# Kernel tuning notes

Hardware: AMD Instinct MI355X
Metric: run time of the kernel (lower is better)

The kernel has to match this reference:

```python
import jax, jax.numpy as jnp
import numpy as np

H = 64
IN_DIM = 32
N = 50000
E = 100000
B = 500


def setup_inputs() -> dict:
    key = jax.random.key(0)
    ks = jax.random.split(key, 16)
    def rn(k, shape, s=0.05):
        return jax.random.normal(k, shape, dtype=jnp.float32) * s
    inp = dict(
        nfeat=rn(ks[0], (N, IN_DIM), 1.0),
        efeat=rn(ks[1], (E, 5), 1.0),
        lin0_w=rn(ks[2], (IN_DIM, H)), lin0_b=jnp.zeros((H,), jnp.float32),
        ew1=rn(ks[3], (5, 128)), eb1=jnp.zeros((128,), jnp.float32),
        ew2=rn(ks[4], (128, H * H)), eb2=jnp.zeros((H * H,), jnp.float32),
        conv_b=jnp.zeros((H,), jnp.float32),
        gru_wih=rn(ks[5], (3 * H, H)), gru_whh=rn(ks[6], (3 * H, H)),
        gru_bih=jnp.zeros((3 * H,), jnp.float32), gru_bhh=jnp.zeros((3 * H,), jnp.float32),
        lstm_wih=rn(ks[7], (4 * H, 2 * H)), lstm_whh=rn(ks[8], (4 * H, H)),
        lstm_bih=jnp.zeros((4 * H,), jnp.float32), lstm_bhh=jnp.zeros((4 * H,), jnp.float32),
        fc1_w=rn(ks[9], (2 * H, H)), fc1_b=jnp.zeros((H,), jnp.float32),
        fc2_w=rn(ks[10], (H, 1)), fc2_b=jnp.zeros((1,), jnp.float32),
        src=jax.random.randint(ks[11], (E,), 0, N),
        dst=jax.random.randint(ks[12], (E,), 0, N),
        graph_id=jnp.arange(N) // (N // B),  # B graphs of equal size, sorted
        num_graphs=B,
    )
    return inp


def reference(nfeat, efeat, lin0_w, lin0_b, ew1, eb1, ew2, eb2, conv_b,
              gru_wih, gru_whh, gru_bih, gru_bhh,
              lstm_wih, lstm_whh, lstm_bih, lstm_bhh,
              fc1_w, fc1_b, fc2_w, fc2_b,
              src, dst, graph_id, num_graphs):
    n_nodes = nfeat.shape[0]
    # lin0 + relu
    h = jax.nn.relu(nfeat @ lin0_w + lin0_b)  # [N, H]
    # edge-conditioned weight matrices (same for all 3 iterations)
    We = (jax.nn.relu(efeat @ ew1 + eb1) @ ew2 + eb2).reshape(-1, H, H)  # [E, H, H]
    deg = jnp.maximum(
        jax.ops.segment_sum(jnp.ones(src.shape[0], jnp.float32), dst, num_segments=n_nodes), 1.0)
    for _ in range(3):
        # NNConv: gather src feats, per-edge matmul, scatter-mean at dst
        msg = jnp.einsum('eh,eho->eo', h[src], We)  # [E, H]
        agg = jax.ops.segment_sum(msg, dst, num_segments=n_nodes) / deg[:, None]
        m = jax.nn.relu(agg + conv_b)
        # GRU step (PyTorch gate order r,z,n)
        gi = m @ gru_wih.T + gru_bih
        gh = h @ gru_whh.T + gru_bhh
        r = jax.nn.sigmoid(gi[:, :H] + gh[:, :H])
        z = jax.nn.sigmoid(gi[:, H:2 * H] + gh[:, H:2 * H])
        n = jnp.tanh(gi[:, 2 * H:] + r * gh[:, 2 * H:])
        h = (1.0 - z) * n + z * h
    feat = h  # [N, H]
    # Set2Set pooling: 3 iters, 1-layer LSTM with input 2H
    q_star = jnp.zeros((num_graphs, 2 * H), jnp.float32)
    hh = jnp.zeros((num_graphs, H), jnp.float32)
    cc = jnp.zeros((num_graphs, H), jnp.float32)
    for _ in range(3):
        gates = q_star @ lstm_wih.T + lstm_bih + hh @ lstm_whh.T + lstm_bhh
        i = jax.nn.sigmoid(gates[:, :H])
        f = jax.nn.sigmoid(gates[:, H:2 * H])
        g = jnp.tanh(gates[:, 2 * H:3 * H])
        o = jax.nn.sigmoid(gates[:, 3 * H:])
        cc = f * cc + i * g
        hh = o * jnp.tanh(cc)
        q = hh  # [B, H]
        e = jnp.sum(feat * q[graph_id], axis=-1)  # [N]
        emax = jax.ops.segment_max(e, graph_id, num_segments=num_graphs)
        alpha = jnp.exp(e - emax[graph_id])
        denom = jax.ops.segment_sum(alpha, graph_id, num_segments=num_graphs)
        alpha = alpha / denom[graph_id]
        readout = jax.ops.segment_sum(alpha[:, None] * feat, graph_id, num_segments=num_graphs)
        q_star = jnp.concatenate([q, readout], axis=-1)  # [B, 2H]
    pred = jax.nn.relu(q_star @ fc1_w + fc1_b) @ fc2_w + fc2_b  # [B, 1]
    return pred.reshape(-1)
```

## Files before the change

kernel.cpp:

```cpp
#include <hip/hip_runtime.h>

#define HD 64
#define NNODE 50000
#define NEDGE 100000
#define NGR 500
#define NPG 100
#define EPAD 100352
#define NCH 66

typedef _Float16 f16;
typedef _Float16 f16x2 __attribute__((ext_vector_type(2)));
typedef _Float16 f16x8 __attribute__((ext_vector_type(8)));
typedef float f32x4 __attribute__((ext_vector_type(4)));

__device__ __forceinline__ float sigmoidf_(float x) { return 1.f / (1.f + __expf(-x)); }

#define G_NODE 12500
#define G_EMLP 392
#define G_GRU  48
#define G_T1   128
#define G_T2   64
#define G_IDX  392
#define G_ALL (G_NODE + G_EMLP + G_GRU + G_T1 + G_T2 + G_IDX)

__global__ __launch_bounds__(256) void k_prep_all(
    const float* __restrict__ nfeat, const float* __restrict__ lin0_w, const float* __restrict__ lin0_b,
    const float* __restrict__ efeat, const float* __restrict__ ew1, const float* __restrict__ eb1,
    const float* __restrict__ gwih, const float* __restrict__ gwhh,
    const float* __restrict__ lwih, const float* __restrict__ lwhh,
    const int* __restrict__ src, const int* __restrict__ dst,
    float* __restrict__ h, f16x2* __restrict__ uP,
    f16* __restrict__ gB1, f16* __restrict__ gB2,
    float* __restrict__ lwihT, float* __restrict__ lwhhT,
    int* __restrict__ srcP, int* __restrict__ dstP, int* __restrict__ cnt) {
    int bb = blockIdx.x;
    int t = threadIdx.x;
    if (bb < G_NODE) {
        int idx = bb * 256 + t;
        int n = idx >> 6, o = idx & 63;
        if (n >= NNODE) return;
        const float* nf = nfeat + n * 32;
        float acc = lin0_b[o];
#pragma unroll
        for (int i = 0; i < 32; i++) acc += nf[i] * lin0_w[i * 64 + o];
        h[idx] = fmaxf(acc, 0.f);
        return;
    }
    bb -= G_NODE;
    if (bb < G_EMLP) {
        __shared__ float sw[5 * 128];
        __shared__ float sb[128];
        for (int idx = t; idx < 640; idx += 256) sw[idx] = ew1[idx];
        if (t < 128) sb[t] = eb1[t];
        __syncthreads();
        int e = bb * 256 + t;
        bool valid = e < NEDGE;
        float ef[5];
#pragma unroll
        for (int i = 0; i < 5; i++) ef[i] = valid ? efeat[e * 5 + i] : 0.f;
#pragma unroll 2
        for (int c = 0; c < 64; c++) {
            float v[2];
#pragma unroll
            for (int s = 0; s < 2; s++) {
                int k = 2 * c + s;
                float acc = sb[k];
#pragma unroll
                for (int i = 0; i < 5; i++) acc += ef[i] * sw[i * 128 + k];
                v[s] = valid ? fmaxf(acc, 0.f) : 0.f;
            }
            f16x2 pv;
            pv[0] = (f16)v[0];
            pv[1] = (f16)v[1];
            uP[(size_t)c * EPAD + e] = pv;
        }
        return;
    }
    bb -= G_EMLP;
    if (bb < G_GRU) {
        int idx = bb * 256 + t;
        int cp = idx >> 6, k = idx & 63;
        int w = cp / 48, rem = cp % 48;
        int tg = rem >> 4, cc = rem & 15;
        int orow = tg * 64 + w * 16 + cc;
        gB1[idx] = (f16)gwih[orow * 64 + k];
        gB2[idx] = (f16)gwhh[orow * 64 + k];
        return;
    }
    bb -= G_GRU;
    if (bb < G_T1) {
        int idx = bb * 256 + t;
        int r = idx >> 7, c = idx & 127;
        lwihT[c * 256 + r] = lwih[idx];
        return;
    }
    bb -= G_T1;
    if (bb < G_T2) {
        int idx = bb * 256 + t;
        int r = idx >> 6, c = idx & 63;
        lwhhT[c * 256 + r] = lwhh[idx];
        return;
    }
    bb -= G_T2;
    {
        int e = bb * 256 + t;
        if (e >= EPAD) return;
        if (e < NEDGE) {
            int d = dst[e];
            srcP[e] = src[e];
            dstP[e] = d;
            atomicAdd(&cnt[d], 1);
        } else {
            srcP[e] = 0;
            dstP[e] = -1;
        }
    }
}

__global__ __launch_bounds__(256) void k_pack_b(const float* __restrict__ ew2,
                                                const float* __restrict__ eb2,
                                                f16* __restrict__ w2hp) {
    __shared__ float s[8192];
    int c = blockIdx.x, t = threadIdx.x;
    for (int i = t; i < 8192; i += 256) {
        int kg = c * 128 + (i >> 6);
        float v = 0.f;
        if (kg < 8192) v = ew2[(size_t)c * 8192 + i];
        else if (kg < 8256) v = eb2[(kg - 8192) * 64 + (i & 63)];
        s[i] = v;
    }
    __syncthreads();
    f16* outp = w2hp + (size_t)c * 8192 + t * 32;
#pragma unroll
    for (int ff = 0; ff < 4; ff++) {
        int F = t * 4 + ff;
        int l = F & 63;
        int jj = (F >> 6) & 3;
        int sl = (F >> 8) & 3;
        f16x8 v;
#pragma unroll
        for (int q = 0; q < 8; q++)
            v[q] = (f16)s[(sl * 32 + ((l >> 4) << 3) + q) * 64 + jj * 16 + (l & 15)];
        *(f16x8*)(outp + ff * 8) = v;
    }
}

#define ISSUEB(BUF, HC)                                                                 \
    {                                                                                   \
        const f16x8* bp = gB + (size_t)(HC) * 512 + l;                                  \
        _Pragma("unroll") for (int s = 0; s < 8; s++) BUF[s] = bp[s * 64];              \
    }
#define COMPH(BUF, BIT)                                                                 \
    {                                                                                   \
        _Pragma("unroll") for (int ks = 0; ks < 2; ks++)                                \
            _Pragma("unroll") for (int i = 0; i < 4; i++) {                             \
                f16x8 av = xf[i][ks] * uc[i][BIT];                                      \
                _Pragma("unroll") for (int j = 0; j < 4; j++)                           \
                    acc[i][j] = __builtin_amdgcn_mfma_f32_16x16x32_f16(av, BUF[ks * 4 + j], acc[i][j], 0, 0, 0); \
            }                                                                           \
    }

__global__ __launch_bounds__(256) void k_msg(
    const float* __restrict__ h, const f16x2* __restrict__ uP, const f16* __restrict__ w2hp,
    const int* __restrict__ srcP, const int* __restrict__ dstP, float* __restrict__ agg) {
    int t = threadIdx.x;
    int w = t >> 6, l = t & 63;
    int eb = blockIdx.x * 256 + w * 64;
    int lr = l & 15, lg = l >> 4;
    f16x8 xf[4][2];
#pragma unroll
    for (int i = 0; i < 4; i++) {
        const float* xb = h + (size_t)srcP[eb + i * 16 + lr] * 64;
#pragma unroll
        for (int p = 0; p < 2; p++) {
            float4 v0 = *(const float4*)(xb + p * 32 + lg * 8);
            float4 v1 = *(const float4*)(xb + p * 32 + lg * 8 + 4);
            f16x8 xv;
            xv[0] = (f16)v0.x; xv[1] = (f16)v0.y; xv[2] = (f16)v0.z; xv[3] = (f16)v0.w;
            xv[4] = (f16)v1.x; xv[5] = (f16)v1.y; xv[6] = (f16)v1.z; xv[7] = (f16)v1.w;
            xf[i][p] = xv;
        }
    }
    const f16x8* gB = (const f16x8*)w2hp;
    f32x4 acc[4][4];
#pragma unroll
    for (int i = 0; i < 4; i++)
#pragma unroll
        for (int j = 0; j < 4; j++) acc[i][j] = (f32x4){0.f, 0.f, 0.f, 0.f};
    f16x8 bA[8], bB[8];
    f16x2 uc[4], un[4];
    ISSUEB(bA, 0)
#pragma unroll
    for (int i = 0; i < 4; i++) uc[i] = uP[eb + i * 16 + lr];
#pragma unroll 1
    for (int c = 0; c < 64; c++) {
        ISSUEB(bB, 2 * c + 1)
        int cn = (c < 63) ? c + 1 : 63;
#pragma unroll
        for (int i = 0; i < 4; i++) un[i] = uP[(size_t)cn * EPAD + eb + i * 16 + lr];
        COMPH(bA, 0)
        ISSUEB(bA, 2 * c + 2)
        COMPH(bB, 1)
#pragma unroll
        for (int i = 0; i < 4; i++) uc[i] = un[i];
        __builtin_amdgcn_s_barrier();
    }
#pragma unroll
    for (int ks = 0; ks < 2; ks++)
#pragma unroll
        for (int i = 0; i < 4; i++)
#pragma unroll
            for (int j = 0; j < 4; j++)
                acc[i][j] = __builtin_amdgcn_mfma_f32_16x16x32_f16(xf[i][ks], bA[ks * 4 + j], acc[i][j], 0, 0, 0);
#pragma unroll
    for (int i = 0; i < 4; i++) {
        int rb = eb + i * 16 + lg * 4;
        int4 d4 = *(const int4*)(dstP + rb);
#pragma unroll
        for (int r = 0; r < 4; r++) {
            int d = (r == 0) ? d4.x : (r == 1) ? d4.y : (r == 2) ? d4.z : d4.w;
            if (d >= 0) {
                float* ap = agg + (size_t)d * 64 + lr;
#pragma unroll
                for (int j = 0; j < 4; j++) atomicAdd(ap + j * 16, acc[i][j][r]);
            }
        }
    }
}

#define GWP 72
__global__ __launch_bounds__(256) void k_gru2(float* __restrict__ agg,
                                              const int* __restrict__ cnt,
                                              const float* __restrict__ convb,
                                              const f16* __restrict__ B1g,
                                              const f16* __restrict__ B2g,
                                              const float* __restrict__ bih,
                                              const float* __restrict__ bhh,
                                              float* __restrict__ h) {
    __shared__ f16 sM[64 * GWP];
    __shared__ f16 sH[64 * GWP];
    int t = threadIdx.x;
    int nb = blockIdx.x * 64;
    int w = t >> 6, l = t & 63, lr = l & 15, lg = l >> 4;
    f16x8 b1[2][3], b2[2][3];
#pragma unroll
    for (int kk = 0; kk < 2; kk++)
#pragma unroll
        for (int j = 0; j < 3; j++) {
            size_t off = (size_t)(w * 48 + j * 16 + lr) * 64 + kk * 32 + lg * 8;
            b1[kk][j] = *(const f16x8*)(B1g + off);
            b2[kk][j] = *(const f16x8*)(B2g + off);
        }
#pragma unroll
    for (int it = 0; it < 16; it++) {
        int idx = t + 256 * it;
        int node = idx >> 6, k = idx & 63;
        int gn = nb + node;
        float mv = 0.f, hv = 0.f;
        if (gn < NNODE) {
            size_t off = (size_t)gn * 64 + k;
            float dinv = 1.f / (float)max(cnt[gn], 1);
            mv = fmaxf(agg[off] * dinv + convb[k], 0.f);
            hv = h[off];
            agg[off] = 0.f;
        }
        sM[node * GWP + k] = (f16)mv;
        sH[node * GWP + k] = (f16)hv;
    }
    __syncthreads();
    f32x4 aih[4][3], ahh[4][3];
#pragma unroll
    for (int i = 0; i < 4; i++)
#pragma unroll
        for (int j = 0; j < 3; j++) {
            aih[i][j] = (f32x4){0.f, 0.f, 0.f, 0.f};
            ahh[i][j] = (f32x4){0.f, 0.f, 0.f, 0.f};
        }
#pragma unroll
    for (int kk = 0; kk < 2; kk++) {
        f16x8 am[4], ah[4];
#pragma unroll
        for (int i = 0; i < 4; i++) {
            am[i] = *(const f16x8*)(sM + (i * 16 + lr) * GWP + kk * 32 + lg * 8);
            ah[i] = *(const f16x8*)(sH + (i * 16 + lr) * GWP + kk * 32 + lg * 8);
        }
#pragma unroll
        for (int i = 0; i < 4; i++)
#pragma unroll
            for (int j = 0; j < 3; j++) {
                aih[i][j] = __builtin_amdgcn_mfma_f32_16x16x32_f16(am[i], b1[kk][j], aih[i][j], 0, 0, 0);
                ahh[i][j] = __builtin_amdgcn_mfma_f32_16x16x32_f16(ah[i], b2[kk][j], ahh[i][j], 0, 0, 0);
            }
    }
    float bi0 = bih[0 * 64 + w * 16 + lr], bh0 = bhh[0 * 64 + w * 16 + lr];
    float bi1 = bih[1 * 64 + w * 16 + lr], bh1 = bhh[1 * 64 + w * 16 + lr];
    float bi2 = bih[2 * 64 + w * 16 + lr], bh2 = bhh[2 * 64 + w * 16 + lr];
#pragma unroll
    for (int i = 0; i < 4; i++)
#pragma unroll
        for (int r = 0; r < 4; r++) {
            int node = i * 16 + lg * 4 + r;
            int gn = nb + node;
            if (gn >= NNODE) continue;
            float rg = sigmoidf_(aih[i][0][r] + bi0 + ahh[i][0][r] + bh0);
            float z = sigmoidf_(aih[i][1][r] + bi1 + ahh[i][1][r] + bh1);
            float nn = tanhf(aih[i][2][r] + bi2 + rg * (ahh[i][2][r] + bh2));
            size_t off = (size_t)gn * 64 + w * 16 + lr;
            float hold = h[off];
            h[off] = (1.f - z) * nn + z * hold;
        }
}

#define FP 68
__global__ __launch_bounds__(256) void k_s2s(const float* __restrict__ feat,
                                             const float* __restrict__ wihT,
                                             const float* __restrict__ whhT,
                                             const float* __restrict__ lbih,
                                             const float* __restrict__ lbhh,
                                             const float* __restrict__ fc1w,
                                             const float* __restrict__ fc1b,
                                             const float* __restrict__ fc2w,
                                             const float* __restrict__ fc2b,
                                             float* __restrict__ out) {
    __shared__ float sf[NPG * FP];
    __shared__ float sq[128];
    __shared__ float sh[64], scc[64];
    __shared__ float sg[256];
    __shared__ float se[NPG];
    __shared__ float red[2];
    int g = blockIdx.x, t = threadIdx.x;
    const float* fb = feat + (size_t)g * NPG * 64;
    for (int idx = t; idx < NPG * 64; idx += 256)
        sf[(idx >> 6) * FP + (idx & 63)] = fb[idx];
    if (t < 128) sq[t] = 0.f;
    if (t >= 128 && t < 192) { sh[t - 128] = 0.f; scc[t - 128] = 0.f; }
    __syncthreads();
    for (int it = 0; it < 3; it++) {
        float gate = lbih[t] + lbhh[t];
#pragma unroll 8
        for (int i = 0; i < 128; i++) gate += sq[i] * wihT[i * 256 + t];
#pragma unroll 8
        for (int i = 0; i < 64; i++) gate += sh[i] * whhT[i * 256 + t];
        sg[t] = gate;
        __syncthreads();
        if (t < 64) {
            float ig = sigmoidf_(sg[t]);
            float fg = sigmoidf_(sg[64 + t]);
            float gg = tanhf(sg[128 + t]);
            float og = sigmoidf_(sg[192 + t]);
            float c = fg * scc[t] + ig * gg;
            scc[t] = c;
            float hv = og * tanhf(c);
            sh[t] = hv;
            sq[t] = hv;
        }
        __syncthreads();
        if (t < NPG) {
            float e = 0.f;
#pragma unroll 8
            for (int o = 0; o < 64; o++) e += sf[t * FP + o] * sh[o];
            se[t] = e;
        }
        __syncthreads();
        if (t < 64) {
            float m = -1e30f;
            for (int i2 = t; i2 < NPG; i2 += 64) m = fmaxf(m, se[i2]);
            for (int d = 32; d; d >>= 1) m = fmaxf(m, __shfl_down(m, d));
            if (t == 0) red[0] = m;
        }
        __syncthreads();
        float emax = red[0];
        if (t < NPG) se[t] = __expf(se[t] - emax);
        __syncthreads();
        if (t < 64) {
            float s = 0.f;
            for (int i2 = t; i2 < NPG; i2 += 64) s += se[i2];
            for (int d = 32; d; d >>= 1) s += __shfl_down(s, d);
            if (t == 0) red[1] = s;
        }
        __syncthreads();
        if (t < 64) {
            float dnv = 1.f / red[1];
            float r = 0.f;
#pragma unroll 4
            for (int n = 0; n < NPG; n++) r += se[n] * sf[n * FP + t];
            sq[64 + t] = r * dnv;
        }
        __syncthreads();
    }
    if (t < 64) {
        float hsum = fc1b[t];
#pragma unroll 8
        for (int i = 0; i < 128; i++) hsum += sq[i] * fc1w[i * 64 + t];
        float p = fmaxf(hsum, 0.f) * fc2w[t];
        for (int d = 32; d; d >>= 1) p += __shfl_down(p, d);
        if (t == 0) out[g] = p + fc2b[0];
    }
}

extern "C" void kernel_launch(void* const* d_in, const int* in_sizes, int n_in,
                              void* d_out, int out_size, void* d_ws, size_t ws_size,
                              hipStream_t stream) {
    const float* nfeat = (const float*)d_in[0];
    const float* efeat = (const float*)d_in[1];
    const float* lin0_w = (const float*)d_in[2];
    const float* lin0_b = (const float*)d_in[3];
    const float* ew1 = (const float*)d_in[4];
    const float* eb1 = (const float*)d_in[5];
    const float* ew2 = (const float*)d_in[6];
    const float* eb2 = (const float*)d_in[7];
    const float* convb = (const float*)d_in[8];
    const float* gwih = (const float*)d_in[9];
    const float* gwhh = (const float*)d_in[10];
    const float* gbih = (const float*)d_in[11];
    const float* gbhh = (const float*)d_in[12];
    const float* lwih = (const float*)d_in[13];
    const float* lwhh = (const float*)d_in[14];
    const float* lbih = (const float*)d_in[15];
    const float* lbhh = (const float*)d_in[16];
    const float* fc1w = (const float*)d_in[17];
    const float* fc1b = (const float*)d_in[18];
    const float* fc2w = (const float*)d_in[19];
    const float* fc2b = (const float*)d_in[20];
    const int* src = (const int*)d_in[21];
    const int* dst = (const int*)d_in[22];
    float* out = (float*)d_out;

    char* p = (char*)d_ws;
    auto alloc = [&](size_t bytes) {
        char* q = p;
        p += (bytes + 255) & ~(size_t)255;
        return q;
    };
    f16x2* uP = (f16x2*)alloc((size_t)64 * EPAD * 4);
    f16* w2hp = (f16*)alloc((size_t)NCH * 8192 * 2);
    float* h = (float*)alloc((size_t)NNODE * 64 * 4);
    float* agg = (float*)alloc((size_t)NNODE * 64 * 4);
    int* cnt = (int*)alloc((size_t)NNODE * 4);
    float* lwihT = (float*)alloc((size_t)128 * 256 * 4);
    float* lwhhT = (float*)alloc((size_t)64 * 256 * 4);
    f16* gB1 = (f16*)alloc((size_t)12288 * 2);
    f16* gB2 = (f16*)alloc((size_t)12288 * 2);
    int* srcP = (int*)alloc((size_t)EPAD * 4);
    int* dstP = (int*)alloc((size_t)EPAD * 4);
    if ((size_t)(p - (char*)d_ws) > ws_size) return;

    hipMemsetAsync(cnt, 0, (size_t)NNODE * 4, stream);
    hipMemsetAsync(agg, 0, (size_t)NNODE * 64 * 4, stream);

    k_prep_all<<<G_ALL, 256, 0, stream>>>(nfeat, lin0_w, lin0_b, efeat, ew1, eb1,
                                          gwih, gwhh, lwih, lwhh, src, dst,
                                          h, uP, gB1, gB2, lwihT, lwhhT, srcP, dstP, cnt);
    k_pack_b<<<NCH, 256, 0, stream>>>(ew2, eb2, w2hp);

    for (int it = 0; it < 3; it++) {
        k_msg<<<EPAD / 256, 256, 0, stream>>>(h, uP, w2hp, srcP, dstP, agg);
        k_gru2<<<(NNODE + 63) / 64, 256, 0, stream>>>(agg, cnt, convb, gB1, gB2, gbih, gbhh, h);
    }
    k_s2s<<<NGR, 256, 0, stream>>>(h, lwihT, lwhhT, lbih, lbhh, fc1w, fc1b, fc2w, fc2b, out);
}
```

Measured before the change: 569.4 us.

## Stage edge-weight B tiles in LDS via async global_load_lds double buffering

The message kernel used to load the per-chunk weight tiles from global memory straight into registers in every wave. It now streams each 16KB chunk into a double-buffered shared-memory tile with global_load_lds, so the four waves share one copy, and reads the fragments from LDS. The bias term is folded into a 65th u-plane of ones, which removes the separate tail MFMA pass. MFMA sections get raised wave priority. The cost is 32KB of LDS per block, which may limit occupancy, plus a full __syncthreads per chunk.

Result: faster. 482.2 us (-15.3%).

```diff
diff --git a/kernel.cpp b/kernel.cpp
--- a/kernel.cpp
+++ b/kernel.cpp
@@ -7,6 +7,7 @@
 #define NPG 100
 #define EPAD 100352
 #define NCH 66
+#define NUPL 65
 
 typedef _Float16 f16;
 typedef _Float16 f16x2 __attribute__((ext_vector_type(2)));
@@ -14,6 +15,11 @@
 typedef float f32x4 __attribute__((ext_vector_type(4)));
 
 __device__ __forceinline__ float sigmoidf_(float x) { return 1.f / (1.f + __expf(-x)); }
+
+__device__ __forceinline__ void gload16(const void* g, void* l) {
+    __builtin_amdgcn_global_load_lds((const __attribute__((address_space(1))) unsigned int*)g,
+                                     (__attribute__((address_space(3))) unsigned int*)l, 16, 0, 0);
+}
 
 #define G_NODE 12500
 #define G_EMLP 392
@@ -74,6 +80,12 @@
             pv[1] = (f16)v[1];
             uP[(size_t)c * EPAD + e] = pv;
         }
+        {
+            f16x2 pv;
+            pv[0] = valid ? (f16)1.f : (f16)0.f;
+            pv[1] = pv[0];
+            uP[(size_t)64 * EPAD + e] = pv;
+        }
         return;
     }
     bb -= G_EMLP;
@@ -145,24 +157,10 @@
     }
 }
 
-#define ISSUEB(BUF, HC)                                                                 \
-    {                                                                                   \
-        const f16x8* bp = gB + (size_t)(HC) * 512 + l;                                  \
-        _Pragma("unroll") for (int s = 0; s < 8; s++) BUF[s] = bp[s * 64];              \
-    }
-#define COMPH(BUF, BIT)                                                                 \
-    {                                                                                   \
-        _Pragma("unroll") for (int ks = 0; ks < 2; ks++)                                \
-            _Pragma("unroll") for (int i = 0; i < 4; i++) {                             \
-                f16x8 av = xf[i][ks] * uc[i][BIT];                                      \
-                _Pragma("unroll") for (int j = 0; j < 4; j++)                           \
-                    acc[i][j] = __builtin_amdgcn_mfma_f32_16x16x32_f16(av, BUF[ks * 4 + j], acc[i][j], 0, 0, 0); \
-            }                                                                           \
-    }
-
 __global__ __launch_bounds__(256) void k_msg(
     const float* __restrict__ h, const f16x2* __restrict__ uP, const f16* __restrict__ w2hp,
     const int* __restrict__ srcP, const int* __restrict__ dstP, float* __restrict__ agg) {
+    __shared__ __attribute__((aligned(16))) f16 sB[2 * 8192];
     int t = threadIdx.x;
     int w = t >> 6, l = t & 63;
     int eb = blockIdx.x * 256 + w * 64;
@@ -182,36 +180,54 @@
         }
     }
     const f16x8* gB = (const f16x8*)w2hp;
+    f16x8* sB8 = (f16x8*)sB;
+#pragma unroll
+    for (int i = 0; i < 4; i++)
+        gload16(gB + i * 256 + w * 64 + l, sB8 + i * 256 + w * 64 + l);
     f32x4 acc[4][4];
 #pragma unroll
     for (int i = 0; i < 4; i++)
 #pragma unroll
         for (int j = 0; j < 4; j++) acc[i][j] = (f32x4){0.f, 0.f, 0.f, 0.f};
-    f16x8 bA[8], bB[8];
     f16x2 uc[4], un[4];
-    ISSUEB(bA, 0)
 #pragma unroll
     for (int i = 0; i < 4; i++) uc[i] = uP[eb + i * 16 + lr];
+    __syncthreads();
 #pragma unroll 1
-    for (int c = 0; c < 64; c++) {
-        ISSUEB(bB, 2 * c + 1)
-        int cn = (c < 63) ? c + 1 : 63;
-#pragma unroll
-        for (int i = 0; i < 4; i++) un[i] = uP[(size_t)cn * EPAD + eb + i * 16 + lr];
-        COMPH(bA, 0)
-        ISSUEB(bA, 2 * c + 2)
-        COMPH(bB, 1)
+    for (int c = 0; c <= 64; c++) {
+        int buf = c & 1;
+        if (c < 64) {
+            const f16x8* gs = gB + (size_t)(c + 1) * 1024;
+            f16x8* ld = sB8 + (buf ^ 1) * 1024;
+#pragma unroll
+            for (int i = 0; i < 4; i++)
+                gload16(gs + i * 256 + w * 64 + l, ld + i * 256 + w * 64 + l);
+            int cn = c + 1;
+#pragma unroll
+            for (int i = 0; i < 4; i++) un[i] = uP[(size_t)cn * EPAD + eb + i * 16 + lr];
+        }
+        f16x8 bf[4][4];
+#pragma unroll
+        for (int s = 0; s < 4; s++)
+#pragma unroll
+            for (int j = 0; j < 4; j++)
+                bf[s][j] = sB8[buf * 1024 + s * 256 + j * 64 + l];
+        __builtin_amdgcn_s_setprio(1);
+#pragma unroll
+        for (int s = 0; s < 4; s++) {
+#pragma unroll
+            for (int i = 0; i < 4; i++) {
+                f16x8 av = xf[i][s & 1] * uc[i][s >> 1];
+#pragma unroll
+                for (int j = 0; j < 4; j++)
+                    acc[i][j] = __builtin_amdgcn_mfma_f32_16x16x32_f16(av, bf[s][j], acc[i][j], 0, 0, 0);
+            }
+        }
+        __builtin_amdgcn_s_setprio(0);
 #pragma unroll
         for (int i = 0; i < 4; i++) uc[i] = un[i];
-        __builtin_amdgcn_s_barrier();
-    }
-#pragma unroll
-    for (int ks = 0; ks < 2; ks++)
-#pragma unroll
-        for (int i = 0; i < 4; i++)
-#pragma unroll
-            for (int j = 0; j < 4; j++)
-                acc[i][j] = __builtin_amdgcn_mfma_f32_16x16x32_f16(xf[i][ks], bA[ks * 4 + j], acc[i][j], 0, 0, 0);
+        __syncthreads();
+    }
 #pragma unroll
     for (int i = 0; i < 4; i++) {
         int rb = eb + i * 16 + lg * 4;
@@ -432,7 +448,7 @@
         p += (bytes + 255) & ~(size_t)255;
         return q;
     };
-    f16x2* uP = (f16x2*)alloc((size_t)64 * EPAD * 4);
+    f16x2* uP = (f16x2*)alloc((size_t)NUPL * EPAD * 4);
     f16* w2hp = (f16*)alloc((size_t)NCH * 8192 * 2);
     float* h = (float*)alloc((size_t)NNODE * 64 * 4);
     float* agg = (float*)alloc((size_t)NNODE * 64 * 4);
```
